# Kernel tuning notes

Measured on AMD Instinct MI355X. Metric: run time of the kernel, lower is better.

## Reference

```python
import jax, jax.numpy as jnp
import numpy as np

B, S, H = 1, 1024, 1024
E, F = 8, 2048
TOP_K = 2


def setup_inputs() -> dict:
    key = jax.random.key(0)
    ks = jax.random.split(key, 5)
    scale = 0.02  # keep activations in a sane range
    return {
        "hidden_states": jax.random.normal(ks[0], (B, S, H), dtype=jnp.float32),
        "gate_w": jax.random.normal(ks[1], (E, H), dtype=jnp.float32) * scale,
        "w1": jax.random.normal(ks[2], (E, F, H), dtype=jnp.float32) * scale,
        "w2": jax.random.normal(ks[3], (E, H, F), dtype=jnp.float32) * scale,
        "w3": jax.random.normal(ks[4], (E, F, H), dtype=jnp.float32) * scale,
    }


def reference(hidden_states, gate_w, w1, w2, w3):
    b, s, h = hidden_states.shape
    x = hidden_states.reshape(-1, h)                      # [T, H]
    T = x.shape[0]

    # Router: logits -> fp32 softmax -> top-k -> renormalize (as in torch code)
    router_logits = x @ gate_w.T                          # [T, E]
    probs = jax.nn.softmax(router_logits.astype(jnp.float32), axis=-1)
    top_w, sel = jax.lax.top_k(probs, TOP_K)              # [T, K]
    top_w = top_w / jnp.sum(top_w, axis=-1, keepdims=True)
    top_w = top_w.astype(x.dtype)

    # Dense combine weights: sum over k of routing_weights * one_hot(sel)
    dense_w = jnp.zeros((T, E), dtype=x.dtype).at[
        jnp.arange(T)[:, None], sel
    ].add(top_w)                                          # [T, E]

    h1 = jnp.einsum("th,efh->tef", x, w1)                 # [T, E, F]
    h3 = jnp.einsum("th,efh->tef", x, w3)
    act = jax.nn.silu(h1) * h3                            # [T, E, F]
    # Weight by routing before the down-projection, then sum over experts
    act_w = act * dense_w[:, :, None]                     # zero for unrouted experts
    out = jnp.einsum("tef,ehf->th", act_w, w2)            # [T, H]

    return out.reshape(b, s, h), router_logits
```

## Files before the change

kernel.cpp:

```cpp
#include <hip/hip_runtime.h>
#include <hip/hip_bf16.h>
#include <cstdint>

#define T_TOK 1024
#define H_DIM 1024
#define F_DIM 2048
#define NE 8
#define BK 32
#define LDT 40
#define NKU (H_DIM / BK)
#define KSPLIT 2
#define KCH (F_DIM / KSPLIT)
#define NKD (KCH / BK)

typedef __attribute__((ext_vector_type(8))) __bf16 bf16x8;
typedef __attribute__((ext_vector_type(4))) float f32x4;

__device__ __forceinline__ ushort f2b(float f) {
    union { float f; uint32_t u; } v; v.f = f;
    uint32_t r = v.u + 0x7FFFu + ((v.u >> 16) & 1u);
    return (ushort)(r >> 16);
}
__device__ __forceinline__ uint32_t pack2(ushort a, ushort b) {
    return (uint32_t)a | ((uint32_t)b << 16);
}
__device__ __forceinline__ uint32_t pkcvt(float a, float b) {
    __hip_bfloat162 h = __float22bfloat162_rn(float2{a, b});
    union { __hip_bfloat162 h; uint32_t u; } c; c.h = h; return c.u;
}

__global__ __launch_bounds__(64) void router_kernel(
    const float* __restrict__ x, const float* __restrict__ gw,
    float* __restrict__ logits_out, ushort* __restrict__ xb,
    int* __restrict__ cnt, int* __restrict__ tlist, float* __restrict__ wlist)
{
    const int t = blockIdx.x;
    const int l = threadIdx.x;
    const float* xr = x + (size_t)t * H_DIM;
    float4 xv[4];
#pragma unroll
    for (int j = 0; j < 4; ++j) xv[j] = ((const float4*)xr)[l * 4 + j];

    {
        uint4 p0, p1;
        p0.x = pkcvt(xv[0].x, xv[0].y);
        p0.y = pkcvt(xv[0].z, xv[0].w);
        p0.z = pkcvt(xv[1].x, xv[1].y);
        p0.w = pkcvt(xv[1].z, xv[1].w);
        p1.x = pkcvt(xv[2].x, xv[2].y);
        p1.y = pkcvt(xv[2].z, xv[2].w);
        p1.z = pkcvt(xv[3].x, xv[3].y);
        p1.w = pkcvt(xv[3].z, xv[3].w);
        uint4* dst = (uint4*)(xb + (size_t)t * H_DIM + l * 16);
        dst[0] = p0; dst[1] = p1;
    }

    float lg[NE];
#pragma unroll
    for (int e = 0; e < NE; ++e) {
        const float* g = gw + (size_t)e * H_DIM;
        float s = 0.f;
#pragma unroll
        for (int j = 0; j < 4; ++j) {
            float4 gv = ((const float4*)g)[l * 4 + j];
            s += xv[j].x * gv.x + xv[j].y * gv.y + xv[j].z * gv.z + xv[j].w * gv.w;
        }
#pragma unroll
        for (int off = 32; off > 0; off >>= 1) s += __shfl_xor(s, off);
        lg[e] = s;
    }
    if (l < NE) logits_out[t * NE + l] = lg[l];

    if (l == 0) {
        int e0 = 0; float m0 = lg[0];
        for (int e = 1; e < NE; ++e) if (lg[e] > m0) { m0 = lg[e]; e0 = e; }
        int e1 = (e0 == 0) ? 1 : 0; float m1 = lg[e1];
        for (int e = 0; e < NE; ++e) if (e != e0 && lg[e] > m1) { m1 = lg[e]; e1 = e; }
        float p1 = __expf(m1 - m0);
        float w0 = 1.f / (1.f + p1);
        float w1v = p1 * w0;
        int p = atomicAdd(&cnt[e0], 1);
        tlist[e0 * T_TOK + p] = t; wlist[e0 * T_TOK + p] = w0;
        p = atomicAdd(&cnt[e1], 1);
        tlist[e1 * T_TOK + p] = t; wlist[e1 * T_TOK + p] = w1v;
    }
}

__global__ void prefix_kernel(const int* __restrict__ cnt, int* __restrict__ aofs) {
    if (threadIdx.x == 0 && blockIdx.x == 0) {
        int o = 0;
        for (int e = 0; e < NE; ++e) { aofs[e] = o; o += ((cnt[e] + 127) >> 7) << 7; }
    }
}

#define PKW(d, s0, s1) { d.x = pkcvt(s0.x, s0.y); d.y = pkcvt(s0.z, s0.w); \
                         d.z = pkcvt(s1.x, s1.y); d.w = pkcvt(s1.z, s1.w); }

__global__ __launch_bounds__(256, 2) void up_kernel(
    const float* __restrict__ w1, const float* __restrict__ w3,
    const ushort* __restrict__ xb,
    const int* __restrict__ cnt, const int* __restrict__ aofs,
    const int* __restrict__ tlist, const float* __restrict__ wlist,
    ushort* __restrict__ act)
{
    const int e = blockIdx.z, tt = blockIdx.y, ft = blockIdx.x;
    const int n = cnt[e];
    if (tt * 128 >= n) return;

    __shared__ int tok[128];
    __shared__ float wt[128];
    __shared__ __align__(16) ushort lds_a[2][128 * LDT];
    __shared__ __align__(16) ushort lds_b1[2][64 * LDT];
    __shared__ __align__(16) ushort lds_b3[2][64 * LDT];

    const int tid = threadIdx.x;
    if (tid < 128) {
        int slot = tt * 128 + tid;
        bool v = slot < n;
        tok[tid] = v ? tlist[e * T_TOK + slot] : 0;
        wt[tid]  = v ? wlist[e * T_TOK + slot] : 0.f;
    }
    __syncthreads();

    const int arow = tid >> 1, aseg = tid & 1;
    const int brow = tid >> 2, bpart = tid & 3;
    const ushort* asrc = xb + (size_t)tok[arow] * H_DIM + aseg * 16;
    const float* b1src = w1 + ((size_t)e * F_DIM + (size_t)ft * 64 + brow) * H_DIM + bpart * 8;
    const float* b3src = w3 + ((size_t)e * F_DIM + (size_t)ft * 64 + brow) * H_DIM + bpart * 8;

    uint4 arA0, arA1, arB0, arB1;
    float4 b1A0, b1A1, b1B0, b1B1;
    float4 b3A0, b3A1, b3B0, b3B1;

#define LOADU(S, k0) { const uint4* s_ = (const uint4*)(asrc + (k0)); \
        ar##S##0 = s_[0]; ar##S##1 = s_[1]; \
        const float4* p1_ = (const float4*)(b1src + (k0)); \
        b1##S##0 = p1_[0]; b1##S##1 = p1_[1]; \
        const float4* p3_ = (const float4*)(b3src + (k0)); \
        b3##S##0 = p3_[0]; b3##S##1 = p3_[1]; }

#define WRITEU(S, buf) { uint4* da_ = (uint4*)&lds_a[buf][arow * LDT + aseg * 16]; \
        da_[0] = ar##S##0; da_[1] = ar##S##1; \
        uint4 pk_; PKW(pk_, b1##S##0, b1##S##1); \
        *(uint4*)&lds_b1[buf][brow * LDT + bpart * 8] = pk_; \
        PKW(pk_, b3##S##0, b3##S##1); \
        *(uint4*)&lds_b3[buf][brow * LDT + bpart * 8] = pk_; }

    const int l = tid & 63, w = tid >> 6;
    const int wm = w >> 1, wn = w & 1;
    const int lr = l & 15, kg = l >> 4;

    f32x4 acc1[4][2], acc3[4][2];
#pragma unroll
    for (int m = 0; m < 4; ++m)
#pragma unroll
        for (int nn = 0; nn < 2; ++nn) {
            acc1[m][nn] = (f32x4){0.f, 0.f, 0.f, 0.f};
            acc3[m][nn] = (f32x4){0.f, 0.f, 0.f, 0.f};
        }

    auto mfma_step = [&](int buf) {
        const ushort* la  = lds_a[buf];
        const ushort* lb1 = lds_b1[buf];
        const ushort* lb3 = lds_b3[buf];
        bf16x8 a[4];
#pragma unroll
        for (int m = 0; m < 4; ++m)
            a[m] = *(const bf16x8*)&la[(wm * 64 + m * 16 + lr) * LDT + kg * 8];
#pragma unroll
        for (int nn = 0; nn < 2; ++nn) {
            bf16x8 b1 = *(const bf16x8*)&lb1[(wn * 32 + nn * 16 + lr) * LDT + kg * 8];
            bf16x8 b3 = *(const bf16x8*)&lb3[(wn * 32 + nn * 16 + lr) * LDT + kg * 8];
#pragma unroll
            for (int m = 0; m < 4; ++m) {
                acc1[m][nn] = __builtin_amdgcn_mfma_f32_16x16x32_bf16(a[m], b1, acc1[m][nn], 0, 0, 0);
                acc3[m][nn] = __builtin_amdgcn_mfma_f32_16x16x32_bf16(a[m], b3, acc3[m][nn], 0, 0, 0);
            }
        }
    };

    LOADU(A, 0);
    WRITEU(A, 0);
    LOADU(B, BK);

    for (int k = 0; k < NKU; k += 2) {
        __syncthreads();
        if (k + 2 < NKU) LOADU(A, (k + 2) * BK);
        mfma_step(0);
        WRITEU(B, 1);
        __syncthreads();
        if (k + 3 < NKU) LOADU(B, (k + 3) * BK);
        mfma_step(1);
        if (k + 2 < NKU) WRITEU(A, 0);
    }
#undef LOADU
#undef WRITEU

    const size_t arow0 = (size_t)aofs[e] + (size_t)tt * 128;
#pragma unroll
    for (int m = 0; m < 4; ++m)
#pragma unroll
        for (int nn = 0; nn < 2; ++nn)
#pragma unroll
            for (int r = 0; r < 4; ++r) {
                int row_local = wm * 64 + m * 16 + kg * 4 + r;
                int col = wn * 32 + nn * 16 + lr;
                float h1 = acc1[m][nn][r], h3 = acc3[m][nn][r];
                float av = (h1 / (1.f + __expf(-h1))) * h3 * wt[row_local];
                act[(arow0 + row_local) * F_DIM + (size_t)ft * 64 + col] = f2b(av);
            }
}

__global__ __launch_bounds__(256, 3) void down_kernel(
    const float* __restrict__ w2, const ushort* __restrict__ act,
    const int* __restrict__ cnt, const int* __restrict__ aofs,
    const int* __restrict__ tlist, float* __restrict__ out)
{
    const int ht = blockIdx.x;
    const int tt = blockIdx.y;
    const int e  = blockIdx.z >> 1;
    const int ks = blockIdx.z & 1;
    const int n = cnt[e];
    if (tt * 128 >= n) return;

    __shared__ int tok[128];
    __shared__ __align__(16) ushort lds_a[2][128 * LDT];
    __shared__ __align__(16) ushort lds_b[2][64 * LDT];

    const int tid = threadIdx.x;
    if (tid < 128) {
        int slot = tt * 128 + tid;
        tok[tid] = (slot < n) ? tlist[e * T_TOK + slot] : -1;
    }
    __syncthreads();

    const int arow = tid >> 1, aseg = tid & 1;
    const int brow = tid >> 2, bpart = tid & 3;
    const ushort* asrc = act + ((size_t)aofs[e] + (size_t)tt * 128 + arow) * F_DIM + ks * KCH + aseg * 16;
    const float*  bsrc = w2 + ((size_t)e * H_DIM + (size_t)ht * 64 + brow) * F_DIM + ks * KCH + bpart * 8;

    uint4 arA0, arA1, arB0, arB1;
    float4 brA0, brA1, brB0, brB1;

#define LOADD(S, k0) { const uint4* s_ = (const uint4*)(asrc + (k0)); \
        ar##S##0 = s_[0]; ar##S##1 = s_[1]; \
        const float4* p_ = (const float4*)(bsrc + (k0)); \
        br##S##0 = p_[0]; br##S##1 = p_[1]; }

#define WRITED(S, buf) { uint4* da_ = (uint4*)&lds_a[buf][arow * LDT + aseg * 16]; \
        da_[0] = ar##S##0; da_[1] = ar##S##1; \
        uint4 pk_; PKW(pk_, br##S##0, br##S##1); \
        *(uint4*)&lds_b[buf][brow * LDT + bpart * 8] = pk_; }

    const int l = tid & 63, w = tid >> 6;
    const int wm = w >> 1, wn = w & 1;
    const int lr = l & 15, kg = l >> 4;

    f32x4 acc[4][2];
#pragma unroll
    for (int m = 0; m < 4; ++m)
#pragma unroll
        for (int nn = 0; nn < 2; ++nn) acc[m][nn] = (f32x4){0.f, 0.f, 0.f, 0.f};

    auto mfma_step = [&](int buf) {
        const ushort* la = lds_a[buf];
        const ushort* lb = lds_b[buf];
        bf16x8 a[4];
#pragma unroll
        for (int m = 0; m < 4; ++m)
            a[m] = *(const bf16x8*)&la[(wm * 64 + m * 16 + lr) * LDT + kg * 8];
#pragma unroll
        for (int nn = 0; nn < 2; ++nn) {
            bf16x8 b = *(const bf16x8*)&lb[(wn * 32 + nn * 16 + lr) * LDT + kg * 8];
#pragma unroll
            for (int m = 0; m < 4; ++m)
                acc[m][nn] = __builtin_amdgcn_mfma_f32_16x16x32_bf16(a[m], b, acc[m][nn], 0, 0, 0);
        }
    };

    LOADD(A, 0);
    WRITED(A, 0);
    LOADD(B, BK);

    for (int k = 0; k < NKD; k += 2) {
        __syncthreads();
        if (k + 2 < NKD) LOADD(A, (k + 2) * BK);
        mfma_step(0);
        WRITED(B, 1);
        __syncthreads();
        if (k + 3 < NKD) LOADD(B, (k + 3) * BK);
        mfma_step(1);
        if (k + 2 < NKD) WRITED(A, 0);
    }
#undef LOADD
#undef WRITED

#pragma unroll
    for (int m = 0; m < 4; ++m)
#pragma unroll
        for (int nn = 0; nn < 2; ++nn)
#pragma unroll
            for (int r = 0; r < 4; ++r) {
                int row_local = wm * 64 + m * 16 + kg * 4 + r;
                int tkn = tok[row_local];
                if (tkn >= 0) {
                    int col = ht * 64 + wn * 32 + nn * 16 + lr;
                    atomicAdd(&out[(size_t)tkn * H_DIM + col], acc[m][nn][r]);
                }
            }
}

extern "C" void kernel_launch(void* const* d_in, const int* in_sizes, int n_in,
                              void* d_out, int out_size, void* d_ws, size_t ws_size,
                              hipStream_t stream) {
    const float* x  = (const float*)d_in[0];
    const float* gw = (const float*)d_in[1];
    const float* w1 = (const float*)d_in[2];
    const float* w2 = (const float*)d_in[3];
    const float* w3 = (const float*)d_in[4];
    float* out = (float*)d_out;
    float* logits = out + (size_t)T_TOK * H_DIM;

    char* ws = (char*)d_ws;
    int*    cnt   = (int*)(ws + 0);
    int*    aofs  = (int*)(ws + 128);
    int*    tlist = (int*)(ws + 4096);
    float*  wlist = (float*)(ws + 4096 + 32768);
    ushort* xb    = (ushort*)(ws + 131072);
    ushort* act   = (ushort*)(ws + (4u << 20));

    hipMemsetAsync(cnt, 0, NE * sizeof(int), stream);
    hipMemsetAsync(out, 0, (size_t)T_TOK * H_DIM * sizeof(float), stream);

    router_kernel<<<dim3(T_TOK), dim3(64), 0, stream>>>(x, gw, logits, xb, cnt, tlist, wlist);
    prefix_kernel<<<dim3(1), dim3(1), 0, stream>>>(cnt, aofs);
    up_kernel<<<dim3(F_DIM / 64, 8, NE), dim3(256), 0, stream>>>(w1, w3, xb, cnt, aofs, tlist, wlist, act);
    down_kernel<<<dim3(H_DIM / 64, 8, NE * KSPLIT), dim3(256), 0, stream>>>(w2, act, cnt, aofs, tlist, out);
}
```

Baseline: 135.1 us.

## Load MFMA operands directly from global memory, dropping LDS staging in expert GEMMs

Both the up-projection and down-projection kernels stop staging tiles through double-buffered shared memory. Each lane now loads its MFMA fragments straight from global memory, converting fp32 weights to bf16 in registers. This removes the LDS writes and reads and the per-step barriers. In exchange, each block reloads data that waves used to share: the A tile is read by both wn waves and the B tile by both wm waves. The row-strided global reads are also less coalesced, and latency is left to the compiler's unroll-4 scheduling and to occupancy.

```diff
diff --git a/kernel.cpp b/kernel.cpp
--- a/kernel.cpp
+++ b/kernel.cpp
@@ -7,11 +7,9 @@
 #define F_DIM 2048
 #define NE 8
 #define BK 32
-#define LDT 40
 #define NKU (H_DIM / BK)
 #define KSPLIT 2
 #define KCH (F_DIM / KSPLIT)
-#define NKD (KCH / BK)
 
 typedef __attribute__((ext_vector_type(8))) __bf16 bf16x8;
 typedef __attribute__((ext_vector_type(4))) float f32x4;
@@ -21,12 +19,15 @@
     uint32_t r = v.u + 0x7FFFu + ((v.u >> 16) & 1u);
     return (ushort)(r >> 16);
 }
-__device__ __forceinline__ uint32_t pack2(ushort a, ushort b) {
-    return (uint32_t)a | ((uint32_t)b << 16);
-}
 __device__ __forceinline__ uint32_t pkcvt(float a, float b) {
     __hip_bfloat162 h = __float22bfloat162_rn(float2{a, b});
     union { __hip_bfloat162 h; uint32_t u; } c; c.h = h; return c.u;
+}
+__device__ __forceinline__ bf16x8 cvt8(float4 a, float4 b) {
+    union { bf16x8 v; uint32_t u[4]; } r;
+    r.u[0] = pkcvt(a.x, a.y); r.u[1] = pkcvt(a.z, a.w);
+    r.u[2] = pkcvt(b.x, b.y); r.u[3] = pkcvt(b.z, b.w);
+    return r.v;
 }
 
 __global__ __launch_bounds__(64) void router_kernel(
@@ -93,9 +94,6 @@
     }
 }
 
-#define PKW(d, s0, s1) { d.x = pkcvt(s0.x, s0.y); d.y = pkcvt(s0.z, s0.w); \
-                         d.z = pkcvt(s1.x, s1.y); d.w = pkcvt(s1.z, s1.w); }
-
 __global__ __launch_bounds__(256, 2) void up_kernel(
     const float* __restrict__ w1, const float* __restrict__ w3,
     const ushort* __restrict__ xb,
@@ -109,10 +107,6 @@
 
     __shared__ int tok[128];
     __shared__ float wt[128];
-    __shared__ __align__(16) ushort lds_a[2][128 * LDT];
-    __shared__ __align__(16) ushort lds_b1[2][64 * LDT];
-    __shared__ __align__(16) ushort lds_b3[2][64 * LDT];
-
     const int tid = threadIdx.x;
     if (tid < 128) {
         int slot = tt * 128 + tid;
@@ -122,34 +116,23 @@
     }
     __syncthreads();
 
-    const int arow = tid >> 1, aseg = tid & 1;
-    const int brow = tid >> 2, bpart = tid & 3;
-    const ushort* asrc = xb + (size_t)tok[arow] * H_DIM + aseg * 16;
-    const float* b1src = w1 + ((size_t)e * F_DIM + (size_t)ft * 64 + brow) * H_DIM + bpart * 8;
-    const float* b3src = w3 + ((size_t)e * F_DIM + (size_t)ft * 64 + brow) * H_DIM + bpart * 8;
-
-    uint4 arA0, arA1, arB0, arB1;
-    float4 b1A0, b1A1, b1B0, b1B1;
-    float4 b3A0, b3A1, b3B0, b3B1;
-
-#define LOADU(S, k0) { const uint4* s_ = (const uint4*)(asrc + (k0)); \
-        ar##S##0 = s_[0]; ar##S##1 = s_[1]; \
-        const float4* p1_ = (const float4*)(b1src + (k0)); \
-        b1##S##0 = p1_[0]; b1##S##1 = p1_[1]; \
-        const float4* p3_ = (const float4*)(b3src + (k0)); \
-        b3##S##0 = p3_[0]; b3##S##1 = p3_[1]; }
-
-#define WRITEU(S, buf) { uint4* da_ = (uint4*)&lds_a[buf][arow * LDT + aseg * 16]; \
-        da_[0] = ar##S##0; da_[1] = ar##S##1; \
-        uint4 pk_; PKW(pk_, b1##S##0, b1##S##1); \
-        *(uint4*)&lds_b1[buf][brow * LDT + bpart * 8] = pk_; \
-        PKW(pk_, b3##S##0, b3##S##1); \
-        *(uint4*)&lds_b3[buf][brow * LDT + bpart * 8] = pk_; }
-
     const int l = tid & 63, w = tid >> 6;
     const int wm = w >> 1, wn = w & 1;
     const int lr = l & 15, kg = l >> 4;
 
+    const ushort* ap[4];
+#pragma unroll
+    for (int m = 0; m < 4; ++m)
+        ap[m] = xb + (size_t)tok[wm * 64 + m * 16 + lr] * H_DIM + kg * 8;
+    const float* b1p[2];
+    const float* b3p[2];
+#pragma unroll
+    for (int nn = 0; nn < 2; ++nn) {
+        size_t row = (size_t)e * F_DIM + (size_t)ft * 64 + wn * 32 + nn * 16 + lr;
+        b1p[nn] = w1 + row * H_DIM + kg * 8;
+        b3p[nn] = w3 + row * H_DIM + kg * 8;
+    }
+
     f32x4 acc1[4][2], acc3[4][2];
 #pragma unroll
     for (int m = 0; m < 4; ++m)
@@ -159,42 +142,27 @@
             acc3[m][nn] = (f32x4){0.f, 0.f, 0.f, 0.f};
         }
 
-    auto mfma_step = [&](int buf) {
-        const ushort* la  = lds_a[buf];
-        const ushort* lb1 = lds_b1[buf];
-        const ushort* lb3 = lds_b3[buf];
+#pragma unroll 4
+    for (int k0 = 0; k0 < H_DIM; k0 += BK) {
         bf16x8 a[4];
 #pragma unroll
         for (int m = 0; m < 4; ++m)
-            a[m] = *(const bf16x8*)&la[(wm * 64 + m * 16 + lr) * LDT + kg * 8];
+            a[m] = *(const bf16x8*)(ap[m] + k0);
 #pragma unroll
         for (int nn = 0; nn < 2; ++nn) {
-            bf16x8 b1 = *(const bf16x8*)&lb1[(wn * 32 + nn * 16 + lr) * LDT + kg * 8];
-            bf16x8 b3 = *(const bf16x8*)&lb3[(wn * 32 + nn * 16 + lr) * LDT + kg * 8];
+            float4 c0 = *(const float4*)(b1p[nn] + k0);
+            float4 c1 = *(const float4*)(b1p[nn] + k0 + 4);
+            bf16x8 bf1 = cvt8(c0, c1);
+            float4 d0 = *(const float4*)(b3p[nn] + k0);
+            float4 d1 = *(const float4*)(b3p[nn] + k0 + 4);
+            bf16x8 bf3 = cvt8(d0, d1);
 #pragma unroll
             for (int m = 0; m < 4; ++m) {
-                acc1[m][nn] = __builtin_amdgcn_mfma_f32_16x16x32_bf16(a[m], b1, acc1[m][nn], 0, 0, 0);
-                acc3[m][nn] = __builtin_amdgcn_mfma_f32_16x16x32_bf16(a[m], b3, acc3[m][nn], 0, 0, 0);
+                acc1[m][nn] = __builtin_amdgcn_mfma_f32_16x16x32_bf16(a[m], bf1, acc1[m][nn], 0, 0, 0);
+                acc3[m][nn] = __builtin_amdgcn_mfma_f32_16x16x32_bf16(a[m], bf3, acc3[m][nn], 0, 0, 0);
             }
         }
-    };
-
-    LOADU(A, 0);
-    WRITEU(A, 0);
-    LOADU(B, BK);
-
-    for (int k = 0; k < NKU; k += 2) {
-        __syncthreads();
-        if (k + 2 < NKU) LOADU(A, (k + 2) * BK);
-        mfma_step(0);
-        WRITEU(B, 1);
-        __syncthreads();
-        if (k + 3 < NKU) LOADU(B, (k + 3) * BK);
-        mfma_step(1);
-        if (k + 2 < NKU) WRITEU(A, 0);
-    }
-#undef LOADU
-#undef WRITEU
+    }
 
     const size_t arow0 = (size_t)aofs[e] + (size_t)tt * 128;
 #pragma unroll
@@ -224,9 +192,6 @@
     if (tt * 128 >= n) return;
 
     __shared__ int tok[128];
-    __shared__ __align__(16) ushort lds_a[2][128 * LDT];
-    __shared__ __align__(16) ushort lds_b[2][64 * LDT];
-
     const int tid = threadIdx.x;
     if (tid < 128) {
         int slot = tt * 128 + tid;
@@ -234,66 +199,45 @@
     }
     __syncthreads();
 
-    const int arow = tid >> 1, aseg = tid & 1;
-    const int brow = tid >> 2, bpart = tid & 3;
-    const ushort* asrc = act + ((size_t)aofs[e] + (size_t)tt * 128 + arow) * F_DIM + ks * KCH + aseg * 16;
-    const float*  bsrc = w2 + ((size_t)e * H_DIM + (size_t)ht * 64 + brow) * F_DIM + ks * KCH + bpart * 8;
-
-    uint4 arA0, arA1, arB0, arB1;
-    float4 brA0, brA1, brB0, brB1;
-
-#define LOADD(S, k0) { const uint4* s_ = (const uint4*)(asrc + (k0)); \
-        ar##S##0 = s_[0]; ar##S##1 = s_[1]; \
-        const float4* p_ = (const float4*)(bsrc + (k0)); \
-        br##S##0 = p_[0]; br##S##1 = p_[1]; }
-
-#define WRITED(S, buf) { uint4* da_ = (uint4*)&lds_a[buf][arow * LDT + aseg * 16]; \
-        da_[0] = ar##S##0; da_[1] = ar##S##1; \
-        uint4 pk_; PKW(pk_, br##S##0, br##S##1); \
-        *(uint4*)&lds_b[buf][brow * LDT + bpart * 8] = pk_; }
-
     const int l = tid & 63, w = tid >> 6;
     const int wm = w >> 1, wn = w & 1;
     const int lr = l & 15, kg = l >> 4;
 
+    const ushort* ap[4];
+#pragma unroll
+    for (int m = 0; m < 4; ++m) {
+        size_t row = (size_t)aofs[e] + (size_t)tt * 128 + wm * 64 + m * 16 + lr;
+        ap[m] = act + row * F_DIM + ks * KCH + kg * 8;
+    }
+    const float* bp[2];
+#pragma unroll
+    for (int nn = 0; nn < 2; ++nn) {
+        size_t row = (size_t)e * H_DIM + (size_t)ht * 64 + wn * 32 + nn * 16 + lr;
+        bp[nn] = w2 + row * F_DIM + ks * KCH + kg * 8;
+    }
+
     f32x4 acc[4][2];
 #pragma unroll
     for (int m = 0; m < 4; ++m)
 #pragma unroll
         for (int nn = 0; nn < 2; ++nn) acc[m][nn] = (f32x4){0.f, 0.f, 0.f, 0.f};
 
-    auto mfma_step = [&](int buf) {
-        const ushort* la = lds_a[buf];
-        const ushort* lb = lds_b[buf];
+#pragma unroll 4
+    for (int k0 = 0; k0 < KCH; k0 += BK) {
         bf16x8 a[4];
 #pragma unroll
         for (int m = 0; m < 4; ++m)
-            a[m] = *(const bf16x8*)&la[(wm * 64 + m * 16 + lr) * LDT + kg * 8];
+            a[m] = *(const bf16x8*)(ap[m] + k0);
 #pragma unroll
         for (int nn = 0; nn < 2; ++nn) {
-            bf16x8 b = *(const bf16x8*)&lb[(wn * 32 + nn * 16 + lr) * LDT + kg * 8];
+            float4 c0 = *(const float4*)(bp[nn] + k0);
+            float4 c1 = *(const float4*)(bp[nn] + k0 + 4);
+            bf16x8 bf = cvt8(c0, c1);
 #pragma unroll
             for (int m = 0; m < 4; ++m)
-                acc[m][nn] = __builtin_amdgcn_mfma_f32_16x16x32_bf16(a[m], b, acc[m][nn], 0, 0, 0);
-        }
-    };
-
-    LOADD(A, 0);
-    WRITED(A, 0);
-    LOADD(B, BK);
-
-    for (int k = 0; k < NKD; k += 2) {
-        __syncthreads();
-        if (k + 2 < NKD) LOADD(A, (k + 2) * BK);
-        mfma_step(0);
-        WRITED(B, 1);
-        __syncthreads();
-        if (k + 3 < NKD) LOADD(B, (k + 3) * BK);
-        mfma_step(1);
-        if (k + 2 < NKD) WRITED(A, 0);
-    }
-#undef LOADD
-#undef WRITED
+                acc[m][nn] = __builtin_amdgcn_mfma_f32_16x16x32_bf16(a[m], bf, acc[m][nn], 0, 0, 0);
+        }
+    }
 
 #pragma unroll
     for (int m = 0; m < 4; ++m)
```

After: 319.5 us. 136% more time.
